# Optimization experiments

Hardware: AMD Instinct MI355X
Metric: run time of the kernel (lower is better)

Reference implementation:

```python
import jax, jax.numpy as jnp
import numpy as np

B, S, D, H = 2, 2048, 2048, 16
HD = D // H


def setup_inputs() -> dict:
    key = jax.random.key(0)
    kx, = jax.random.split(key, 1)
    return {
        "x": jax.random.normal(kx, (B, S, D), dtype=jnp.float32),
        "q_mask": jnp.ones((D, D), dtype=jnp.float32),
        "k_mask": jnp.ones((D, D), dtype=jnp.float32),
        "v_mask": jnp.ones((D, D), dtype=jnp.float32),
        "out_mask": jnp.ones((D, D), dtype=jnp.float32),
        "head_mask": jnp.ones((H,), dtype=jnp.float32),
        "attention_mask": jnp.ones((B, S), dtype=jnp.float32),
        "shared_weight": jnp.float32(1.0),
    }


def reference(x, q_mask, k_mask, v_mask, out_mask, head_mask, attention_mask, shared_weight):
    b, s, d = x.shape
    scale = jnp.float32(HD) ** -0.5

    def shared_linear(inp, mask):
        # F.linear(x, mask * shared_weight): out = inp @ (mask*sw).T
        return jnp.einsum("bsd,ed->bse", inp, mask * shared_weight)

    q = shared_linear(x, q_mask).reshape(b, s, H, HD).transpose(0, 2, 1, 3)  # [B,H,S,HD]
    k = shared_linear(x, k_mask).reshape(b, s, H, HD).transpose(0, 2, 1, 3)
    v = shared_linear(x, v_mask).reshape(b, s, H, HD).transpose(0, 2, 1, 3)

    hm = head_mask.reshape(1, H, 1, 1)
    q, k, v = q * hm, k * hm, v * hm

    scores = jnp.einsum("bhqd,bhkd->bhqk", q, k) * scale  # [B,H,S,S]

    # causal mask: upper triangle (j > i) -> -inf
    causal = jnp.triu(jnp.ones((s, s), dtype=bool), k=1)
    scores = jnp.where(causal, -jnp.inf, scores)

    # additive attention mask: (1 - m) * -10000, broadcast [B,1,1,S]
    scores = scores + (1.0 - attention_mask)[:, None, None, :] * -10000.0

    attn = jax.nn.softmax(scores, axis=-1)  # dropout is identity in eval / p=0

    out = jnp.einsum("bhqk,bhkd->bhqd", attn, v)          # [B,H,S,HD]
    out = out.transpose(0, 2, 1, 3).reshape(b, s, d)       # [B,S,D]
    return shared_linear(out, out_mask)
```

## Files before the change

kernel.cpp:

```cpp
#include <hip/hip_runtime.h>

#define B_  2
#define S_  2048
#define D_  2048
#define H_  16
#define HD_ 128

typedef __bf16 bf16;
typedef __bf16 bf16x4 __attribute__((ext_vector_type(4)));
typedef __bf16 bf16x8 __attribute__((ext_vector_type(8)));
typedef float  f32x4  __attribute__((ext_vector_type(4)));
typedef unsigned int u32x4 __attribute__((ext_vector_type(4)));

__device__ __forceinline__ void gld_lds16(const void* g, void* l) {
    __builtin_amdgcn_global_load_lds(
        (const __attribute__((address_space(1))) unsigned int*)g,
        (__attribute__((address_space(3))) unsigned int*)l, 16, 0, 0);
}

__device__ __forceinline__ f32x4 mfma16(bf16x8 a, bf16x8 b, f32x4 c) {
    return __builtin_amdgcn_mfma_f32_16x16x32_bf16(a, b, c, 0, 0, 0);
}

#define BAR()        asm volatile("s_barrier" ::: "memory")
#define WAIT_LGKM0() do { asm volatile("s_waitcnt lgkmcnt(0)" ::: "memory"); \
                          __builtin_amdgcn_sched_barrier(0); } while (0)

__global__ __launch_bounds__(256)
void precast_kernel(const float* __restrict__ x, bf16* __restrict__ xh,
                    bf16* __restrict__ xl) {
    int i = (blockIdx.x * 256 + threadIdx.x) * 8;
    float4 a = *(const float4*)(x + i);
    float4 b = *(const float4*)(x + i + 4);
    float av[8] = {a.x, a.y, a.z, a.w, b.x, b.y, b.z, b.w};
    bf16x8 h8, l8;
#pragma unroll
    for (int e = 0; e < 8; e++) {
        bf16 hv = (bf16)av[e];
        h8[e] = hv;
        l8[e] = (bf16)(av[e] - (float)hv);
    }
    *(bf16x8*)(xh + i) = h8;
    *(bf16x8*)(xl + i) = l8;
}

__global__ __launch_bounds__(256)
void precast_mask(const float* __restrict__ s0, bf16* __restrict__ d0,
                  const float* __restrict__ s1, bf16* __restrict__ d1,
                  const float* __restrict__ swp) {
    const float sw = swp[0];
    int bid = blockIdx.x;
    const float* src = s0; bf16* dst = d0;
    if (bid >= 2048) { src = s1; dst = d1; bid -= 2048; }
    int i = (bid * 256 + threadIdx.x) * 8;
    float4 a = *(const float4*)(src + i);
    float4 b = *(const float4*)(src + i + 4);
    bf16x8 o;
    o[0] = (bf16)(a.x * sw); o[1] = (bf16)(a.y * sw);
    o[2] = (bf16)(a.z * sw); o[3] = (bf16)(a.w * sw);
    o[4] = (bf16)(b.x * sw); o[5] = (bf16)(b.y * sw);
    o[6] = (bf16)(b.z * sw); o[7] = (bf16)(b.w * sw);
    *(bf16x8*)(dst + i) = o;
}

template<int BM, int BN, int MODE>
__global__ __launch_bounds__(256, 2)
void gemm2p(const bf16* __restrict__ Ah_g, const bf16* __restrict__ Al_g,
            const bf16* __restrict__ Bq, const bf16* __restrict__ Bk,
            const float* __restrict__ hm,
            bf16* __restrict__ o_qh, bf16* __restrict__ o_ql,
            bf16* __restrict__ o_kh, bf16* __restrict__ o_kl,
            bf16* __restrict__ o_vt, float* __restrict__ o_f32,
            int nt) {
    constexpr int IM = BM / 2 / 16;
    constexpr int JN = BN / 2 / 16;
    constexpr int IH = IM / 2;
    constexpr int ISSA = BM / 64;
    constexpr int ISSB = BN / 64;
    constexpr int BUFE = (BM + BN) * 32;
    constexpr int SMELEMS = (MODE == 1 && BN * (BM + 8) > 2 * BUFE)
                                ? BN * (BM + 8) : 2 * BUFE;
    __shared__ bf16 sm[SMELEMS];

    const int t = threadIdx.x;
    const int wave = t >> 6, lane = t & 63;
    const int lrow = lane & 15, quad = lane >> 4;
    const int wr = wave >> 1, wc = wave & 1;

    const int gx = gridDim.x;
    const int id0 = blockIdx.y * gx + blockIdx.x;
    const int nwg = gx * gridDim.y;
    const int id = (id0 & 7) * (nwg >> 3) + (id0 >> 3);
    const int m0 = (id / gx) * BM, n0 = (id % gx) * BN;

    const int nsec = (MODE == 0) ? (n0 & (D_ - 1)) : n0;
    const bf16* Bg = (MODE == 0 && n0 >= D_) ? Bk : Bq;

    const int arow = wr * (BM / 2) + lrow;
    const int brow = wc * (BN / 2) + lrow;
    const int gsw = (quad ^ ((lrow >> 1) & 3)) * 8;

    const int srr = lane >> 2, spg = lane & 3;
    const int ssw = (spg ^ ((srr >> 1) & 3)) * 8;

    auto stage_A = [&](int kt, int pbuf) {
        const bf16* As = (MODE == 0 && kt >= 64) ? Al_g : Ah_g;
        const int kc = ((MODE == 0) ? (kt & 63) : kt) * 32;
        bf16* buf = sm + pbuf * BUFE;
#pragma unroll
        for (int pp = 0; pp < ISSA; pp++) {
            int r0 = wave * (BM / 4) + pp * 16;
            gld_lds16(As + (size_t)(m0 + r0 + srr) * D_ + kc + ssw,
                      buf + r0 * 32);
        }
    };
    auto stage_B = [&](int kt, int pbuf) {
        const int kc = ((MODE == 0) ? (kt & 63) : kt) * 32;
        bf16* buf = sm + pbuf * BUFE + BM * 32;
#pragma unroll
        for (int pp = 0; pp < ISSB; pp++) {
            int r0 = wave * (BN / 4) + pp * 16;
            gld_lds16(Bg + (size_t)(nsec + r0 + srr) * D_ + kc + ssw,
                      buf + r0 * 32);
        }
    };

    f32x4 acc[IM][JN];
#pragma unroll
    for (int i = 0; i < IM; i++)
#pragma unroll
        for (int j = 0; j < JN; j++) acc[i][j] = (f32x4){0.f, 0.f, 0.f, 0.f};

    stage_A(0, 0); stage_B(0, 0); stage_B(1, 1);

    int p = 0;
    for (int kt = 0; kt < nt; ++kt) {
        if (kt < nt - 1) asm volatile("s_waitcnt vmcnt(2)" ::: "memory");
        else             asm volatile("s_waitcnt vmcnt(0)" ::: "memory");
        BAR();
        if (kt + 1 < nt) stage_A(kt + 1, p ^ 1);

        const bf16* Ab = sm + p * BUFE;
        const bf16* Bb = Ab + BM * 32;
        bf16x8 a[IH], b[JN];

#pragma unroll
        for (int j = 0; j < JN; j++)
            b[j] = *(const bf16x8*)&Bb[(brow + j * 16) * 32 + gsw];
#pragma unroll
        for (int i = 0; i < IH; i++)
            a[i] = *(const bf16x8*)&Ab[(arow + i * 16) * 32 + gsw];
        BAR();
        WAIT_LGKM0();
        __builtin_amdgcn_s_setprio(1);
#pragma unroll
        for (int i = 0; i < IH; i++)
#pragma unroll
            for (int j = 0; j < JN; j++)
                acc[i][j] = mfma16(a[i], b[j], acc[i][j]);
        __builtin_amdgcn_s_setprio(0);
        BAR();

        if (kt + 2 < nt) stage_B(kt + 2, p);

#pragma unroll
        for (int i = 0; i < IH; i++)
            a[i] = *(const bf16x8*)&Ab[(arow + (IH + i) * 16) * 32 + gsw];
        WAIT_LGKM0();
        __builtin_amdgcn_s_setprio(1);
#pragma unroll
        for (int i = 0; i < IH; i++)
#pragma unroll
            for (int j = 0; j < JN; j++)
                acc[IH + i][j] = mfma16(a[i], b[j], acc[IH + i][j]);
        __builtin_amdgcn_s_setprio(0);
        p ^= 1;
    }

    if constexpr (MODE == 0) {
        const bool isq = (n0 < D_);
        bf16* oh = isq ? o_qh : o_kh;
        bf16* ol = isq ? o_ql : o_kl;
#pragma unroll
        for (int j = 0; j < JN; j++) {
            int nb = nsec + wc * (BN / 2) + j * 16;
            int h = nb >> 7;
            float hv = hm[h];
#pragma unroll
            for (int i = 0; i < IM; i++) {
                int mB = m0 + wr * (BM / 2) + i * 16 + quad * 4;
                int bb = mB >> 11, s = mB & (S_ - 1);
                size_t idx0 = (((size_t)bb * H_ + h) * S_ + s) * HD_ + (nb & 127) + lrow;
#pragma unroll
                for (int r = 0; r < 4; r++) {
                    float v = acc[i][j][r] * hv;
                    bf16 hvv = (bf16)v;
                    bf16 lvv = (bf16)(v - (float)hvv);
                    oh[idx0 + (size_t)r * HD_] = hvv;
                    ol[idx0 + (size_t)r * HD_] = lvv;
                }
            }
        }
    }
    if constexpr (MODE == 1) {
        __syncthreads();
        bf16* tr = sm;
#pragma unroll
        for (int j = 0; j < JN; j++) {
            int nl = wc * (BN / 2) + j * 16 + lrow;
            float hv = hm[(n0 + nl) >> 7];
#pragma unroll
            for (int i = 0; i < IM; i++) {
                int ml = wr * (BM / 2) + i * 16 + quad * 4;
                bf16x4 pk;
#pragma unroll
                for (int r = 0; r < 4; r++) pk[r] = (bf16)(acc[i][j][r] * hv);
                *(bf16x4*)&tr[nl * 136 + ml] = pk;
            }
        }
        __syncthreads();
        const int bI = m0 >> 11;
        const int s0 = m0 & (S_ - 1);
#pragma unroll
        for (int w = 0; w < 8; w++) {
            int nrow = w * 16 + (t >> 4);
            int c = t & 15;
            bf16x8 vv = *(const bf16x8*)&tr[nrow * 136 + c * 8];
            int ng = n0 + nrow;
            int h = ng >> 7, hd = ng & 127;
            *(bf16x8*)&o_vt[((size_t)(bI * H_ + h) * HD_ + hd) * S_ + s0 + c * 8] = vv;
        }
    }
    if constexpr (MODE == 2) {
#pragma unroll
        for (int j = 0; j < JN; j++) {
            int n = n0 + wc * (BN / 2) + j * 16 + lrow;
#pragma unroll
            for (int i = 0; i < IM; i++) {
                int mB = m0 + wr * (BM / 2) + i * 16 + quad * 4;
#pragma unroll
                for (int r = 0; r < 4; r++)
                    o_f32[(size_t)(mB + r) * D_ + n] = acc[i][j][r];
            }
        }
    }
}

#define SPLD 72

__global__ __launch_bounds__(256, 2)
void attn_kernel(const bf16* __restrict__ qh_, const bf16* __restrict__ ql_,
                 const bf16* __restrict__ kh_, const bf16* __restrict__ kl_,
                 const bf16* __restrict__ vt_, const float* __restrict__ am,
                 bf16* __restrict__ outp) {
    const int bh = blockIdx.x & 31;
    const int qblk = 31 - (blockIdx.x >> 5);
    const int b = bh >> 4, h = bh & 15;
    const int i0 = qblk * 64;
    const int t = threadIdx.x, wave = t >> 6, lane = t & 63;
    const int lrow = lane & 15, quad = lane >> 4;

    __shared__ bf16 skh[64 * 128];
    __shared__ bf16 skl[64 * 128];
    __shared__ bf16 svt[128 * 64];
    __shared__ bf16 sp[4][16 * SPLD];

    const size_t kbase = (size_t)bh * S_ * HD_;
    const size_t vbase = (size_t)bh * HD_ * S_;

    const int qrow = i0 + wave * 16 + lrow;
    bf16x8 qhf[4], qlf[4];
#pragma unroll
    for (int c = 0; c < 4; c++) {
        qhf[c] = *(const bf16x8*)&qh_[kbase + (size_t)qrow * HD_ + c * 32 + quad * 8];
        qlf[c] = *(const bf16x8*)&ql_[kbase + (size_t)qrow * HD_ + c * 32 + quad * 8];
    }

    u32x4 kpre[8], vpre[4];
    auto issueKV = [&](int j0) {
#pragma unroll
        for (int p = 0; p < 4; p++) {
            int rb = wave * 16 + p * 4;
            int r = rb + (lane >> 4);
            int gl = ((lane & 15) ^ (r & 7)) * 8;
            kpre[p]     = *(const u32x4*)(kh_ + kbase + (size_t)(j0 + r) * HD_ + gl);
            kpre[4 + p] = *(const u32x4*)(kl_ + kbase + (size_t)(j0 + r) * HD_ + gl);
        }
#pragma unroll
        for (int p = 0; p < 4; p++) {
            int db = wave * 32 + p * 8;
            int d = db + (lane >> 3);
            int gl = ((lane & 7) ^ (d & 7)) * 8;
            vpre[p] = *(const u32x4*)(vt_ + vbase + (size_t)d * S_ + j0 + gl);
        }
    };
    auto writeKV = [&]() {
#pragma unroll
        for (int p = 0; p < 4; p++) {
            int rb = wave * 16 + p * 4;
            *(u32x4*)&skh[rb * 128 + lane * 8] = kpre[p];
            *(u32x4*)&skl[rb * 128 + lane * 8] = kpre[4 + p];
        }
#pragma unroll
        for (int p = 0; p < 4; p++) {
            int db = wave * 32 + p * 8;
            *(u32x4*)&svt[db * 64 + lane * 8] = vpre[p];
        }
    };

    float m_i[4], l_i[4];
    f32x4 O[8];
#pragma unroll
    for (int r = 0; r < 4; r++) { m_i[r] = -INFINITY; l_i[r] = 0.f; }
#pragma unroll
    for (int n2 = 0; n2 < 8; n2++) O[n2] = (f32x4){0.f, 0.f, 0.f, 0.f};

    const float scale = 0.08838834764831845f;

    issueKV(0);

    for (int j0 = 0; j0 <= i0; j0 += 64) {
        asm volatile("s_waitcnt vmcnt(0)" ::: "memory");
        BAR();
        writeKV();
        if (j0 + 64 <= i0) issueKV(j0 + 64);
        asm volatile("s_waitcnt lgkmcnt(0)" ::: "memory");
        BAR();

        float amadd[4];
#pragma unroll
        for (int nt = 0; nt < 4; nt++)
            amadd[nt] = (1.0f - am[b * S_ + j0 + nt * 16 + lrow]) * -10000.0f;

        f32x4 s4[4];
#pragma unroll
        for (int nt = 0; nt < 4; nt++) s4[nt] = (f32x4){0.f, 0.f, 0.f, 0.f};
#pragma unroll
        for (int c = 0; c < 4; c++) {
#pragma unroll
            for (int nt = 0; nt < 4; nt++) {
                int ka = (nt * 16 + lrow) * 128 + (((c * 4 + quad) ^ (lrow & 7)) * 8);
                bf16x8 kb8 = *(const bf16x8*)&skh[ka];
                bf16x8 lb8 = *(const bf16x8*)&skl[ka];
                s4[nt] = mfma16(qhf[c], kb8, s4[nt]);
                s4[nt] = mfma16(qhf[c], lb8, s4[nt]);
                s4[nt] = mfma16(qlf[c], kb8, s4[nt]);
            }
        }

        const bool diag = (j0 == i0);
#pragma unroll
        for (int r = 0; r < 4; r++) {
            const int rrow = wave * 16 + quad * 4 + r;
            float sv[4], pw[4];
            float mx = -INFINITY;
#pragma unroll
            for (int nt = 0; nt < 4; nt++) {
                float xv = s4[nt][r] * scale + amadd[nt];
                if (diag && (nt * 16 + lrow) > rrow) xv = -INFINITY;
                sv[nt] = xv;
                mx = fmaxf(mx, xv);
            }
#pragma unroll
            for (int off = 1; off < 16; off <<= 1) mx = fmaxf(mx, __shfl_xor(mx, off));
            float mnew = fmaxf(m_i[r], mx);
            float alpha = __expf(m_i[r] - mnew);
            float ps = 0.f;
#pragma unroll
            for (int nt = 0; nt < 4; nt++) { pw[nt] = __expf(sv[nt] - mnew); ps += pw[nt]; }
#pragma unroll
            for (int off = 1; off < 16; off <<= 1) ps += __shfl_xor(ps, off);
            l_i[r] = l_i[r] * alpha + ps;
            m_i[r] = mnew;
#pragma unroll
            for (int n2 = 0; n2 < 8; n2++) O[n2][r] *= alpha;
#pragma unroll
            for (int nt = 0; nt < 4; nt++)
                sp[wave][(quad * 4 + r) * SPLD + nt * 16 + lrow] = (bf16)pw[nt];
        }
        asm volatile("s_waitcnt lgkmcnt(0)" ::: "memory");

#pragma unroll
        for (int k2 = 0; k2 < 2; k2++) {
            bf16x8 pf = *(const bf16x8*)&sp[wave][lrow * SPLD + k2 * 32 + quad * 8];
            const int gp = ((quad + k2 * 4) ^ (lrow & 7)) * 8;
#pragma unroll
            for (int n2 = 0; n2 < 8; n2++) {
                bf16x8 vf8 = *(const bf16x8*)&svt[(n2 * 16 + lrow) * 64 + gp];
                O[n2] = mfma16(pf, vf8, O[n2]);
            }
        }
    }

    float inv[4];
#pragma unroll
    for (int r = 0; r < 4; r++) inv[r] = 1.0f / l_i[r];
#pragma unroll
    for (int n2 = 0; n2 < 8; n2++)
#pragma unroll
        for (int r = 0; r < 4; r++) {
            int srow = i0 + wave * 16 + quad * 4 + r;
            outp[((size_t)(b * S_ + srow)) * D_ + h * HD_ + n2 * 16 + lrow] =
                (bf16)(O[n2][r] * inv[r]);
        }
}

extern "C" void kernel_launch(void* const* d_in, const int* in_sizes, int n_in,
                              void* d_out, int out_size, void* d_ws, size_t ws_size,
                              hipStream_t stream) {
    const float* x  = (const float*)d_in[0];
    const float* qm = (const float*)d_in[1];
    const float* km = (const float*)d_in[2];
    const float* vm = (const float*)d_in[3];
    const float* om = (const float*)d_in[4];
    const float* hm = (const float*)d_in[5];
    const float* am = (const float*)d_in[6];
    const float* sw = (const float*)d_in[7];
    float* out = (float*)d_out;

    const size_t P = (size_t)B_ * H_ * S_ * HD_ * sizeof(bf16);
    char* ws = (char*)d_ws;
    bf16* xh = (bf16*)(ws + 0 * P);
    bf16* xl = (bf16*)(ws + 1 * P);
    bf16* qh = (bf16*)(ws + 2 * P);
    bf16* ql = (bf16*)(ws + 3 * P);
    bf16* kh = (bf16*)(ws + 4 * P);
    bf16* kl = (bf16*)(ws + 5 * P);
    bf16* attn_out = xh;
    bf16* vmb = xl;
    bf16* omb = qh;
    bf16* vt  = (bf16*)d_out;
    bf16* qmb = (bf16*)((char*)d_out + 16u * 1024 * 1024);
    bf16* kmb = (bf16*)((char*)d_out + 24u * 1024 * 1024);

    precast_kernel<<<4096, 256, 0, stream>>>(x, xh, xl);
    precast_mask<<<4096, 256, 0, stream>>>(qm, qmb, km, kmb, sw);

    gemm2p<256, 128, 0><<<dim3(32, 16), 256, 0, stream>>>(
        xh, xl, qmb, kmb, hm, qh, ql, kh, kl, nullptr, nullptr, 128);

    precast_mask<<<2048, 256, 0, stream>>>(vm, vmb, nullptr, nullptr, sw);
    gemm2p<128, 128, 1><<<dim3(16, 32), 256, 0, stream>>>(
        xh, nullptr, vmb, nullptr, hm,
        nullptr, nullptr, nullptr, nullptr, vt, nullptr, 64);

    attn_kernel<<<1024, 256, 0, stream>>>(qh, ql, kh, kl, vt, am, attn_out);

    precast_mask<<<2048, 256, 0, stream>>>(om, omb, nullptr, nullptr, sw);
    gemm2p<128, 128, 2><<<dim3(16, 32), 256, 0, stream>>>(
        attn_out, nullptr, omb, nullptr, hm,
        nullptr, nullptr, nullptr, nullptr, nullptr, out, 64);
}
```

Before: 491.5 us.

## Prefetch both A halves early in GEMM, add MFMA priority, merge precasts

Inside the GEMM main loop, the LDS reads for the second half of A now go out together with the first half. A partial lgkmcnt wait replaces the mid-iteration barrier plus full wait, so the later LDS reads overlap the first MFMA block. The attention kernel gets s_setprio raised around its MFMA loops. The x precast and the q/k mask precasts are merged into a single launch to cut launch overhead. The trade-off is higher register pressure from holding both A fragments at once.

```diff
diff --git a/kernel.cpp b/kernel.cpp
--- a/kernel.cpp
+++ b/kernel.cpp
@@ -22,36 +22,36 @@
     return __builtin_amdgcn_mfma_f32_16x16x32_bf16(a, b, c, 0, 0, 0);
 }
 
-#define BAR()        asm volatile("s_barrier" ::: "memory")
-#define WAIT_LGKM0() do { asm volatile("s_waitcnt lgkmcnt(0)" ::: "memory"); \
-                          __builtin_amdgcn_sched_barrier(0); } while (0)
+#define BAR()  asm volatile("s_barrier" ::: "memory")
+#define SBAR() __builtin_amdgcn_sched_barrier(0)
 
 __global__ __launch_bounds__(256)
-void precast_kernel(const float* __restrict__ x, bf16* __restrict__ xh,
-                    bf16* __restrict__ xl) {
-    int i = (blockIdx.x * 256 + threadIdx.x) * 8;
-    float4 a = *(const float4*)(x + i);
-    float4 b = *(const float4*)(x + i + 4);
-    float av[8] = {a.x, a.y, a.z, a.w, b.x, b.y, b.z, b.w};
-    bf16x8 h8, l8;
-#pragma unroll
-    for (int e = 0; e < 8; e++) {
-        bf16 hv = (bf16)av[e];
-        h8[e] = hv;
-        l8[e] = (bf16)(av[e] - (float)hv);
-    }
-    *(bf16x8*)(xh + i) = h8;
-    *(bf16x8*)(xl + i) = l8;
-}
-
-__global__ __launch_bounds__(256)
-void precast_mask(const float* __restrict__ s0, bf16* __restrict__ d0,
-                  const float* __restrict__ s1, bf16* __restrict__ d1,
-                  const float* __restrict__ swp) {
+void precast_all(const float* __restrict__ x, bf16* __restrict__ xh,
+                 bf16* __restrict__ xl,
+                 const float* __restrict__ qm, bf16* __restrict__ qmb,
+                 const float* __restrict__ km, bf16* __restrict__ kmb,
+                 const float* __restrict__ swp) {
+    int bid = blockIdx.x;
+    if (bid < 4096) {
+        int i = (bid * 256 + threadIdx.x) * 8;
+        float4 a = *(const float4*)(x + i);
+        float4 b = *(const float4*)(x + i + 4);
+        float av[8] = {a.x, a.y, a.z, a.w, b.x, b.y, b.z, b.w};
+        bf16x8 h8, l8;
+#pragma unroll
+        for (int e = 0; e < 8; e++) {
+            bf16 hv = (bf16)av[e];
+            h8[e] = hv;
+            l8[e] = (bf16)(av[e] - (float)hv);
+        }
+        *(bf16x8*)(xh + i) = h8;
+        *(bf16x8*)(xl + i) = l8;
+        return;
+    }
     const float sw = swp[0];
-    int bid = blockIdx.x;
-    const float* src = s0; bf16* dst = d0;
-    if (bid >= 2048) { src = s1; dst = d1; bid -= 2048; }
+    bid -= 4096;
+    const float* src = qm; bf16* dst = qmb;
+    if (bid >= 2048) { src = km; dst = kmb; bid -= 2048; }
     int i = (bid * 256 + threadIdx.x) * 8;
     float4 a = *(const float4*)(src + i);
     float4 b = *(const float4*)(src + i + 4);
@@ -61,6 +61,21 @@
     o[4] = (bf16)(b.x * sw); o[5] = (bf16)(b.y * sw);
     o[6] = (bf16)(b.z * sw); o[7] = (bf16)(b.w * sw);
     *(bf16x8*)(dst + i) = o;
+}
+
+__global__ __launch_bounds__(256)
+void precast_mask(const float* __restrict__ s0, bf16* __restrict__ d0,
+                  const float* __restrict__ swp) {
+    const float sw = swp[0];
+    int i = (blockIdx.x * 256 + threadIdx.x) * 8;
+    float4 a = *(const float4*)(s0 + i);
+    float4 b = *(const float4*)(s0 + i + 4);
+    bf16x8 o;
+    o[0] = (bf16)(a.x * sw); o[1] = (bf16)(a.y * sw);
+    o[2] = (bf16)(a.z * sw); o[3] = (bf16)(a.w * sw);
+    o[4] = (bf16)(b.x * sw); o[5] = (bf16)(b.y * sw);
+    o[6] = (bf16)(b.z * sw); o[7] = (bf16)(b.w * sw);
+    *(bf16x8*)(d0 + i) = o;
 }
 
 template<int BM, int BN, int MODE>
@@ -142,37 +157,41 @@
 
         const bf16* Ab = sm + p * BUFE;
         const bf16* Bb = Ab + BM * 32;
-        bf16x8 a[IH], b[JN];
+        bf16x8 b[JN], au[IH], al[IH];
 
 #pragma unroll
         for (int j = 0; j < JN; j++)
             b[j] = *(const bf16x8*)&Bb[(brow + j * 16) * 32 + gsw];
 #pragma unroll
         for (int i = 0; i < IH; i++)
-            a[i] = *(const bf16x8*)&Ab[(arow + i * 16) * 32 + gsw];
-        BAR();
-        WAIT_LGKM0();
+            au[i] = *(const bf16x8*)&Ab[(arow + i * 16) * 32 + gsw];
+        SBAR();
+#pragma unroll
+        for (int i = 0; i < IH; i++)
+            al[i] = *(const bf16x8*)&Ab[(arow + (IH + i) * 16) * 32 + gsw];
+        SBAR();
+        if constexpr (IH == 4) asm volatile("s_waitcnt lgkmcnt(4)" ::: "memory");
+        else                   asm volatile("s_waitcnt lgkmcnt(2)" ::: "memory");
+        SBAR();
         __builtin_amdgcn_s_setprio(1);
 #pragma unroll
         for (int i = 0; i < IH; i++)
 #pragma unroll
             for (int j = 0; j < JN; j++)
-                acc[i][j] = mfma16(a[i], b[j], acc[i][j]);
+                acc[i][j] = mfma16(au[i], b[j], acc[i][j]);
         __builtin_amdgcn_s_setprio(0);
         BAR();
 
         if (kt + 2 < nt) stage_B(kt + 2, p);
 
+        asm volatile("s_waitcnt lgkmcnt(0)" ::: "memory");
+        SBAR();
+        __builtin_amdgcn_s_setprio(1);
 #pragma unroll
         for (int i = 0; i < IH; i++)
-            a[i] = *(const bf16x8*)&Ab[(arow + (IH + i) * 16) * 32 + gsw];
-        WAIT_LGKM0();
-        __builtin_amdgcn_s_setprio(1);
-#pragma unroll
-        for (int i = 0; i < IH; i++)
 #pragma unroll
             for (int j = 0; j < JN; j++)
-                acc[IH + i][j] = mfma16(a[i], b[j], acc[IH + i][j]);
+                acc[IH + i][j] = mfma16(al[i], b[j], acc[IH + i][j]);
         __builtin_amdgcn_s_setprio(0);
         p ^= 1;
     }
@@ -335,6 +354,7 @@
         f32x4 s4[4];
 #pragma unroll
         for (int nt = 0; nt < 4; nt++) s4[nt] = (f32x4){0.f, 0.f, 0.f, 0.f};
+        __builtin_amdgcn_s_setprio(1);
 #pragma unroll
         for (int c = 0; c < 4; c++) {
 #pragma unroll
@@ -347,6 +367,7 @@
                 s4[nt] = mfma16(qlf[c], kb8, s4[nt]);
             }
         }
+        __builtin_amdgcn_s_setprio(0);
 
         const bool diag = (j0 == i0);
 #pragma unroll
@@ -380,6 +401,7 @@
         }
         asm volatile("s_waitcnt lgkmcnt(0)" ::: "memory");
 
+        __builtin_amdgcn_s_setprio(1);
 #pragma unroll
         for (int k2 = 0; k2 < 2; k2++) {
             bf16x8 pf = *(const bf16x8*)&sp[wave][lrow * SPLD + k2 * 32 + quad * 8];
@@ -390,6 +412,7 @@
                 O[n2] = mfma16(pf, vf8, O[n2]);
             }
         }
+        __builtin_amdgcn_s_setprio(0);
     }
 
     float inv[4];
@@ -433,20 +456,19 @@
     bf16* qmb = (bf16*)((char*)d_out + 16u * 1024 * 1024);
     bf16* kmb = (bf16*)((char*)d_out + 24u * 1024 * 1024);
 
-    precast_kernel<<<4096, 256, 0, stream>>>(x, xh, xl);
-    precast_mask<<<4096, 256, 0, stream>>>(qm, qmb, km, kmb, sw);
+    precast_all<<<8192, 256, 0, stream>>>(x, xh, xl, qm, qmb, km, kmb, sw);
 
     gemm2p<256, 128, 0><<<dim3(32, 16), 256, 0, stream>>>(
         xh, xl, qmb, kmb, hm, qh, ql, kh, kl, nullptr, nullptr, 128);
 
-    precast_mask<<<2048, 256, 0, stream>>>(vm, vmb, nullptr, nullptr, sw);
+    precast_mask<<<2048, 256, 0, stream>>>(vm, vmb, sw);
     gemm2p<128, 128, 1><<<dim3(16, 32), 256, 0, stream>>>(
         xh, nullptr, vmb, nullptr, hm,
         nullptr, nullptr, nullptr, nullptr, vt, nullptr, 64);
 
     attn_kernel<<<1024, 256, 0, stream>>>(qh, ql, kh, kl, vt, am, attn_out);
 
-    precast_mask<<<2048, 256, 0, stream>>>(om, omb, nullptr, nullptr, sw);
+    precast_mask<<<2048, 256, 0, stream>>>(om, omb, sw);
     gemm2p<128, 128, 2><<<dim3(16, 32), 256, 0, stream>>>(
         attn_out, nullptr, omb, nullptr, hm,
         nullptr, nullptr, nullptr, nullptr, nullptr, out, 64);
```

Result: no change. 490.6 us (-0.2%).
